# Kernel optimization log

Hardware: AMD Instinct MI355X
Metric: run time of the kernel (lower is better)

The kernel has to match this reference:

```python
import jax, jax.numpy as jnp
import numpy as np

B, S, E, H, G = 2, 2048, 2048, 16, 4
D = E // H  # head dim = 128


def setup_inputs() -> dict:
    key = jax.random.key(0)
    ks = jax.random.split(key, 7)
    scale = 1.0 / np.sqrt(E)
    x = jax.random.normal(ks[0], (B, S, E), dtype=jnp.float32)
    Wq = jax.random.normal(ks[1], (H, E, D), dtype=jnp.float32) * scale
    bq = jax.random.normal(ks[2], (H, D), dtype=jnp.float32) * 0.02
    Wk = jax.random.normal(ks[3], (G, E, D), dtype=jnp.float32) * scale
    bk = jax.random.normal(ks[4], (G, D), dtype=jnp.float32) * 0.02
    Wv = jax.random.normal(ks[5], (G, E, D), dtype=jnp.float32) * scale
    bv = jax.random.normal(ks[6], (G, D), dtype=jnp.float32) * 0.02
    return {"x": x, "Wq": Wq, "bq": bq, "Wk": Wk, "bk": bk, "Wv": Wv, "bv": bv}


def reference(x, Wq, bq, Wk, bk, Wv, bv):
    # x: [B,S,E]; Wq: [H,E,D]; Wk/Wv: [G,E,D]
    h, e, d = Wq.shape
    g = Wk.shape[0]
    per = h // g  # Q heads per KV group
    s = x.shape[1]

    # batched QKV projections (replaces per-head nn.Linear loop)
    q = jnp.einsum('bse,hed->bhsd', x, Wq) + bq[None, :, None, :]   # [B,H,S,D]
    kg = jnp.einsum('bse,ged->bgsd', x, Wk) + bk[None, :, None, :]  # [B,G,S,D]
    vg = jnp.einsum('bse,ged->bgsd', x, Wv) + bv[None, :, None, :]

    # GQA: each KV group serves `per` consecutive Q heads (order i*per+j)
    k = jnp.repeat(kg, per, axis=1)  # [B,H,S,D]
    v = jnp.repeat(vg, per, axis=1)

    scores = jnp.einsum('bhqd,bhkd->bhqk', q, k) * (1.0 / np.sqrt(d))
    causal = jnp.triu(jnp.ones((s, s), dtype=bool), k=1)  # strict upper = masked
    scores = jnp.where(causal[None, None, :, :], -jnp.inf, scores)
    attn = jax.nn.softmax(scores, axis=-1)
    out = jnp.einsum('bhqk,bhkd->bhqd', attn, v)  # [B,H,S,D]
    # concat per-head outputs along feature dim (head order matches loop order)
    return out.transpose(0, 2, 1, 3).reshape(x.shape[0], s, h * d)
```

## Files before the change

kernel.cpp:

```cpp
#include <hip/hip_runtime.h>
#include <hip/hip_bf16.h>
#include <math.h>


typedef __attribute__((ext_vector_type(8))) short bf16x8;
typedef __attribute__((ext_vector_type(4))) short s16x4;
typedef __attribute__((ext_vector_type(4))) float f32x4;
typedef __attribute__((ext_vector_type(16))) float f32x16;

#define LOG2E 1.4426950408889634f

__device__ __forceinline__ short f2bf(float f) {
  union { float f; unsigned u; } v; v.f = f;
  unsigned r = v.u + 0x7FFFu + ((v.u >> 16) & 1u);
  return (short)(r >> 16);
}

__device__ __forceinline__ short hwbf(float f) {
  __hip_bfloat16 h = __float2bfloat16(f);
  return *(short*)&h;
}

__device__ __forceinline__ unsigned pkbf(float a, float b) {
  return (unsigned)(unsigned short)hwbf(a) | ((unsigned)(unsigned short)hwbf(b) << 16);
}

__device__ __forceinline__ void async16(const void* g, void* l) {
  __builtin_amdgcn_global_load_lds(
      (const __attribute__((address_space(1))) void*)g,
      (__attribute__((address_space(3))) void*)l, 16, 0, 0);
}

__device__ __forceinline__ f32x4 mfma16(bf16x8 a, bf16x8 b, f32x4 c) {
  return __builtin_amdgcn_mfma_f32_16x16x32_bf16(a, b, c, 0, 0, 0);
}

__device__ __forceinline__ f32x16 mfma32(bf16x8 a, bf16x8 b, f32x16 c) {
  return __builtin_amdgcn_mfma_f32_32x32x16_bf16(a, b, c, 0, 0, 0);
}


__global__ void conv_x(const float4* __restrict__ x, s16x4* __restrict__ xb) {
  const int i = blockIdx.x * 256 + threadIdx.x;
  float4 v = x[i];
  s16x4 o;
  o[0] = f2bf(v.x); o[1] = f2bf(v.y); o[2] = f2bf(v.z); o[3] = f2bf(v.w);
  xb[i] = o;
}

__global__ void transpose_w(const float* __restrict__ src, short* __restrict__ wt, int c0) {
  __shared__ float t[32][33];
  const int hh = blockIdx.z;
  const int e0 = blockIdx.x * 32, d0 = blockIdx.y * 32;
  const int tx = threadIdx.x, ty = threadIdx.y;
  const float* s = src + (size_t)hh * 2048 * 128;
#pragma unroll
  for (int i = ty; i < 32; i += 8)
    t[i][tx] = s[(size_t)(e0 + i) * 128 + d0 + tx];
  __syncthreads();
#pragma unroll
  for (int i = ty; i < 32; i += 8)
    wt[(size_t)(c0 + hh * 128 + d0 + i) * 2048 + e0 + tx] = f2bf(t[tx][i]);
}

__global__ void build_bias(const float* __restrict__ bq, const float* __restrict__ bk,
                           const float* __restrict__ bv, float* __restrict__ bc) {
  const int c = blockIdx.x * 256 + threadIdx.x;
  float v;
  if (c < 2048)      v = bq[c];
  else if (c < 2560) v = bk[c - 2048];
  else               v = bv[c - 2560];
  bc[c] = v;
}


__global__ __launch_bounds__(256) void qkv_gemm(
    const short* __restrict__ xb, const short* __restrict__ wt,
    const float* __restrict__ bc,
    short* __restrict__ qb, short* __restrict__ kb, short* __restrict__ vt)
{
  constexpr int E = 2048, BK = 32;
  __shared__ short Al[2][128 * BK];
  __shared__ short Bl[2][128 * BK];
  const int tid = threadIdx.x;
  const int lane = tid & 63, wave = tid >> 6;
  const int wr = wave >> 1, wc = wave & 1;
  const int l16 = lane & 15, grp = lane >> 4;
  const int work = (blockIdx.x & 7) * 96 + (blockIdx.x >> 3);
  const int m0 = (work / 24) * 128, n0 = (work % 24) * 128;

  const int c1 = tid, c2 = tid + 256;
  const int r1 = c1 >> 2, s1 = c1 & 3, r2 = c2 >> 2, s2 = c2 & 3;

  f32x4 acc[4][4] = {};

  async16(xb + (size_t)(m0 + r1) * E + s1 * 8, (char*)Al[0] + c1 * 16);
  async16(xb + (size_t)(m0 + r2) * E + s2 * 8, (char*)Al[0] + c2 * 16);
  async16(wt + (size_t)(n0 + r1) * E + s1 * 8, (char*)Bl[0] + c1 * 16);
  async16(wt + (size_t)(n0 + r2) * E + s2 * 8, (char*)Bl[0] + c2 * 16);
  __syncthreads();

  const int nk = E / BK;
  for (int t = 0; t < nk; ++t) {
    const int cur = t & 1;
    if (t + 1 < nk) {
      const int k0 = (t + 1) * BK;
      async16(xb + (size_t)(m0 + r1) * E + k0 + s1 * 8, (char*)Al[cur ^ 1] + c1 * 16);
      async16(xb + (size_t)(m0 + r2) * E + k0 + s2 * 8, (char*)Al[cur ^ 1] + c2 * 16);
      async16(wt + (size_t)(n0 + r1) * E + k0 + s1 * 8, (char*)Bl[cur ^ 1] + c1 * 16);
      async16(wt + (size_t)(n0 + r2) * E + k0 + s2 * 8, (char*)Bl[cur ^ 1] + c2 * 16);
    }
    bf16x8 af[4], bfr[4];
#pragma unroll
    for (int mi = 0; mi < 4; ++mi)
      af[mi] = *(const bf16x8*)&Al[cur][(wr * 64 + mi * 16 + l16) * BK + grp * 8];
#pragma unroll
    for (int ni = 0; ni < 4; ++ni)
      bfr[ni] = *(const bf16x8*)&Bl[cur][(wc * 64 + ni * 16 + l16) * BK + grp * 8];
#pragma unroll
    for (int mi = 0; mi < 4; ++mi)
#pragma unroll
      for (int ni = 0; ni < 4; ++ni)
        acc[mi][ni] = mfma16(af[mi], bfr[ni], acc[mi][ni]);
    __syncthreads();
  }

  const float qscale = 0.08838834764831845f;
#pragma unroll
  for (int ni = 0; ni < 4; ++ni) {
    const int c = n0 + wc * 64 + ni * 16 + l16;
    const float bias = bc[c];
    const int d = c & 127;
#pragma unroll
    for (int mi = 0; mi < 4; ++mi) {
      const int rbase = m0 + wr * 64 + mi * 16 + grp * 4;
      const int b = rbase >> 11;
      const int s = rbase & 2047;
      f32x4 a = acc[mi][ni];
      if (c < 2048) {
        const int h = c >> 7;
        short* dst = qb + ((size_t)(b * 16 + h) * 2048 + s) * 128 + d;
#pragma unroll
        for (int r = 0; r < 4; ++r) dst[(size_t)r * 128] = f2bf((a[r] + bias) * qscale);
      } else if (c < 2560) {
        const int gi = (c >> 7) & 3;
        short* dst = kb + ((size_t)(b * 4 + gi) * 2048 + s) * 128 + d;
#pragma unroll
        for (int r = 0; r < 4; ++r) dst[(size_t)r * 128] = f2bf(a[r] + bias);
      } else {
        const int gi = (c >> 7) & 3;
        s16x4 pk;
#pragma unroll
        for (int r = 0; r < 4; ++r) pk[r] = f2bf(a[r] + bias);
        const int vcol = (s & ~12) | ((s & 4) << 1) | ((s & 8) >> 1);
        *(s16x4*)&vt[((size_t)(b * 4 + gi) * 128 + d) * 2048 + vcol] = pk;
      }
    }
  }
}


__device__ __forceinline__ void stageKV(char* kd, char* vd,
                                        const short* __restrict__ Kg,
                                        const short* __restrict__ Vg,
                                        int kv0, int tid) {
#pragma unroll
  for (int rd = 0; rd < 4; ++rd) {
    const int off = rd * 4096 + tid * 16;
    const int row = off >> 8, colb = off & 255;
    const int sc = colb ^ ((row & 15) << 4);
    async16(Kg + (size_t)(kv0 + row) * 128 + (sc >> 1), kd + off);
  }
#pragma unroll
  for (int rd = 0; rd < 4; ++rd) {
    const int off = rd * 4096 + tid * 16;
    const int row = off >> 7, colb = off & 127;
    const int sc = colb ^ ((row & 7) << 4);
    async16(Vg + (size_t)row * 2048 + kv0 + (sc >> 1), vd + off);
  }
}

__global__ __launch_bounds__(256) void attn(
    const short* __restrict__ qb, const short* __restrict__ kb,
    const short* __restrict__ vt, float* __restrict__ out)
{
  constexpr int S = 2048, D = 128;
  extern __shared__ char lds[];
  const int tid = threadIdx.x;
  const int lane = tid & 63, wave = tid >> 6;
  const int l32 = lane & 31;
  const int hhf = lane >> 5;
  const int swzK = (l32 & 15) << 4;
  const int swzV = (l32 & 7) << 4;
  const int work = (blockIdx.x & 7) * 32 + (blockIdx.x >> 3);
  const int bg = work >> 5;
  const int b = bg >> 2, g = bg & 3;
  const int h = g * 4 + ((work >> 3) & 3);
  const int x = work & 7;

  const short* Qg = qb + (size_t)(b * 16 + h) * S * D;
  const short* Kg = kb + (size_t)(b * 4 + g) * S * D;
  const short* Vg = vt + (size_t)(b * 4 + g) * (size_t)D * S;

#pragma unroll
  for (int p = 0; p < 2; ++p) {
    const int jj = p ? (15 - x) : x;
    const int q0 = jj * 128 + wave * 32;
    const int nt = 2 * (jj + 1);

    bf16x8 qf[8];
#pragma unroll
    for (int c = 0; c < 8; ++c)
      qf[c] = *(const bf16x8*)&Qg[(size_t)(q0 + l32) * D + c * 16 + hhf * 8];

    f32x16 o[4] = {};
    float mrun = -INFINITY, lrun = 0.f;

    stageKV(lds, lds + 32768, Kg, Vg, 0, tid);
    __syncthreads();

    for (int t = 0; t < nt; ++t) {
      const int kv0 = t << 6;
      const int cur = t & 1;
      if (t + 1 < nt)
        stageKV(lds + (cur ^ 1) * 16384, lds + 32768 + (cur ^ 1) * 16384,
                Kg, Vg, kv0 + 64, tid);
      const char* Kb = lds + cur * 16384;
      const char* Vb = lds + 32768 + cur * 16384;

      if (kv0 <= q0 + 31) {
        f32x16 st[2] = {};
        __builtin_amdgcn_s_setprio(1);
#pragma unroll
        for (int c = 0; c < 8; ++c) {
          const int X = c * 32 + hhf * 16;
          bf16x8 k0 = *(const bf16x8*)(Kb + (size_t)l32 * 256 + (X ^ swzK));
          st[0] = mfma32(k0, qf[c], st[0]);
          bf16x8 k1 = *(const bf16x8*)(Kb + (size_t)(32 + l32) * 256 + (X ^ swzK));
          st[1] = mfma32(k1, qf[c], st[1]);
        }
        __builtin_amdgcn_s_setprio(0);

        if (kv0 + 63 > q0) {
          const int qa = q0 + l32;
#pragma unroll
          for (int r = 0; r < 16; ++r) {
            const int kl = (r & 3) + 8 * (r >> 2) + 4 * hhf;
            if (kv0 + kl > qa)      st[0][r] = -INFINITY;
            if (kv0 + 32 + kl > qa) st[1][r] = -INFINITY;
          }
        }

        float tmax = -INFINITY;
#pragma unroll
        for (int r = 0; r < 16; ++r) {
          tmax = fmaxf(tmax, st[0][r]);
          tmax = fmaxf(tmax, st[1][r]);
        }
        tmax = fmaxf(tmax, __shfl_xor(tmax, 32));
        float fac = 1.0f;
        if (!__all(tmax <= mrun + 8.0f)) {
          const float mn = fmaxf(mrun, tmax);
          fac = exp2f((mrun - mn) * LOG2E);
#pragma unroll
          for (int db = 0; db < 4; ++db) o[db] *= fac;
          mrun = mn;
        }
        float lsum = 0.f;
        float ps0[16], ps1[16];
#pragma unroll
        for (int r = 0; r < 16; ++r) {
          ps0[r] = exp2f((st[0][r] - mrun) * LOG2E); lsum += ps0[r];
          ps1[r] = exp2f((st[1][r] - mrun) * LOG2E); lsum += ps1[r];
        }
        lsum += __shfl_xor(lsum, 32);
        lrun = lrun * fac + lsum;

        bf16x8 pf[4];
#pragma unroll
        for (int kbi = 0; kbi < 4; ++kbi) {
          union { unsigned u[4]; bf16x8 v; } tu;
          const int c0 = 8 * (kbi & 1);
          if (kbi < 2) {
            tu.u[0] = pkbf(ps0[c0 + 0], ps0[c0 + 1]);
            tu.u[1] = pkbf(ps0[c0 + 2], ps0[c0 + 3]);
            tu.u[2] = pkbf(ps0[c0 + 4], ps0[c0 + 5]);
            tu.u[3] = pkbf(ps0[c0 + 6], ps0[c0 + 7]);
          } else {
            tu.u[0] = pkbf(ps1[c0 + 0], ps1[c0 + 1]);
            tu.u[1] = pkbf(ps1[c0 + 2], ps1[c0 + 3]);
            tu.u[2] = pkbf(ps1[c0 + 4], ps1[c0 + 5]);
            tu.u[3] = pkbf(ps1[c0 + 6], ps1[c0 + 7]);
          }
          pf[kbi] = tu.v;
        }

        __builtin_amdgcn_s_setprio(1);
#pragma unroll
        for (int kbi = 0; kbi < 4; ++kbi) {
          const int X = kbi * 32 + hhf * 16;
#pragma unroll
          for (int db = 0; db < 4; ++db) {
            bf16x8 vf = *(const bf16x8*)(Vb + (size_t)(db * 32 + l32) * 128 + (X ^ swzV));
            o[db] = mfma32(vf, pf[kbi], o[db]);
          }
        }
        __builtin_amdgcn_s_setprio(0);
      }
      __syncthreads();
    }

    const float inv = 1.f / lrun;
    float* orow = out + ((size_t)b * S + q0 + l32) * 2048 + h * D;
#pragma unroll
    for (int db = 0; db < 4; ++db)
#pragma unroll
      for (int rq = 0; rq < 4; ++rq) {
        f32x4 w;
        w[0] = o[db][4 * rq + 0] * inv;
        w[1] = o[db][4 * rq + 1] * inv;
        w[2] = o[db][4 * rq + 2] * inv;
        w[3] = o[db][4 * rq + 3] * inv;
        *(f32x4*)&orow[db * 32 + 8 * rq + 4 * hhf] = w;
      }
  }
}


extern "C" void kernel_launch(void* const* d_in, const int* in_sizes, int n_in,
                              void* d_out, int out_size, void* d_ws, size_t ws_size,
                              hipStream_t stream) {
  const float* x  = (const float*)d_in[0];
  const float* Wq = (const float*)d_in[1];
  const float* bq = (const float*)d_in[2];
  const float* Wk = (const float*)d_in[3];
  const float* bk = (const float*)d_in[4];
  const float* Wv = (const float*)d_in[5];
  const float* bv = (const float*)d_in[6];
  float* out = (float*)d_out;

  char* ws = (char*)d_ws;
  short* xb = (short*)ws;
  short* wt = (short*)(ws + (size_t)16 * 1024 * 1024);
  float* bc = (float*)(ws + (size_t)28 * 1024 * 1024);
  short* qb = (short*)(ws + (size_t)28 * 1024 * 1024 + 65536);
  short* kb = (short*)((char*)qb + (size_t)16 * 1024 * 1024);
  short* vt = (short*)((char*)kb + (size_t)4 * 1024 * 1024);

  conv_x<<<8192, 256, 0, stream>>>((const float4*)x, (s16x4*)xb);
  dim3 tb(32, 8);
  transpose_w<<<dim3(64, 4, 16), tb, 0, stream>>>(Wq, wt, 0);
  transpose_w<<<dim3(64, 4, 4),  tb, 0, stream>>>(Wk, wt, 2048);
  transpose_w<<<dim3(64, 4, 4),  tb, 0, stream>>>(Wv, wt, 2560);
  build_bias<<<12, 256, 0, stream>>>(bq, bk, bv, bc);
  qkv_gemm<<<768, 256, 0, stream>>>(xb, wt, bc, qb, kb, vt);

  (void)hipFuncSetAttribute((const void*)attn, hipFuncAttributeMaxDynamicSharedMemorySize, 65536);
  attn<<<256, 256, 65536, stream>>>(qb, kb, vt, out);
}
```

Before: 267.2 us.

## Triple-buffer K/V tiles in attention with explicit vmcnt waits

Moves the attention kernel's K/V LDS staging from double to triple buffering. Tiles are now prefetched two iterations ahead, and __syncthreads is replaced by raw s_barrier plus partial s_waitcnt vmcnt counts, so the next tile's global loads can stay in flight while the current tile is consumed. This is meant to hide global memory latency better. In exchange LDS use grows from 64KB to 96KB per block, and correctness now depends on hand-counted outstanding-load numbers.

```diff
diff --git a/kernel.cpp b/kernel.cpp
--- a/kernel.cpp
+++ b/kernel.cpp
@@ -160,7 +160,7 @@
 }
 
 
-__device__ __forceinline__ void stageKV(char* kd, char* vd,
+__device__ __forceinline__ void stageKV(char* set,
                                         const short* __restrict__ Kg,
                                         const short* __restrict__ Vg,
                                         int kv0, int tid) {
@@ -169,14 +169,14 @@
     const int off = rd * 4096 + tid * 16;
     const int row = off >> 8, colb = off & 255;
     const int sc = colb ^ ((row & 15) << 4);
-    async16(Kg + (size_t)(kv0 + row) * 128 + (sc >> 1), kd + off);
+    async16(Kg + (size_t)(kv0 + row) * 128 + (sc >> 1), set + off);
   }
 #pragma unroll
   for (int rd = 0; rd < 4; ++rd) {
     const int off = rd * 4096 + tid * 16;
     const int row = off >> 7, colb = off & 127;
     const int sc = colb ^ ((row & 7) << 4);
-    async16(Vg + (size_t)row * 2048 + kv0 + (sc >> 1), vd + off);
+    async16(Vg + (size_t)row * 2048 + kv0 + (sc >> 1), set + 16384 + off);
   }
 }
 
@@ -216,17 +216,28 @@
     f32x16 o[4] = {};
     float mrun = -INFINITY, lrun = 0.f;
 
-    stageKV(lds, lds + 32768, Kg, Vg, 0, tid);
-    __syncthreads();
-
+    __builtin_amdgcn_s_barrier();
+    stageKV(lds, Kg, Vg, 0, tid);
+    stageKV(lds + 32768, Kg, Vg, 64, tid);
+
+    int cb = 0;
+    int sb = 2;
     for (int t = 0; t < nt; ++t) {
       const int kv0 = t << 6;
-      const int cur = t & 1;
-      if (t + 1 < nt)
-        stageKV(lds + (cur ^ 1) * 16384, lds + 32768 + (cur ^ 1) * 16384,
-                Kg, Vg, kv0 + 64, tid);
-      const char* Kb = lds + cur * 16384;
-      const char* Vb = lds + 32768 + cur * 16384;
+      __builtin_amdgcn_s_barrier();
+      if (t + 2 < nt) {
+        stageKV(lds + sb * 32768, Kg, Vg, kv0 + 128, tid);
+        asm volatile("s_waitcnt vmcnt(16)" ::: "memory");
+      } else if (t + 1 < nt) {
+        asm volatile("s_waitcnt vmcnt(8)" ::: "memory");
+      } else {
+        asm volatile("s_waitcnt vmcnt(0)" ::: "memory");
+      }
+      __builtin_amdgcn_s_barrier();
+      __builtin_amdgcn_sched_barrier(0);
+
+      const char* Kb = lds + cb * 32768;
+      const char* Vb = lds + cb * 32768 + 16384;
 
       if (kv0 <= q0 + 31) {
         f32x16 st[2] = {};
@@ -307,7 +318,8 @@
         }
         __builtin_amdgcn_s_setprio(0);
       }
-      __syncthreads();
+      cb = (cb == 2) ? 0 : cb + 1;
+      sb = (sb == 2) ? 0 : sb + 1;
     }
 
     const float inv = 1.f / lrun;
@@ -355,6 +367,6 @@
   build_bias<<<12, 256, 0, stream>>>(bq, bk, bv, bc);
   qkv_gemm<<<768, 256, 0, stream>>>(xb, wt, bc, qb, kb, vt);
 
-  (void)hipFuncSetAttribute((const void*)attn, hipFuncAttributeMaxDynamicSharedMemorySize, 65536);
-  attn<<<256, 256, 65536, stream>>>(qb, kb, vt, out);
-}
+  (void)hipFuncSetAttribute((const void*)attn, hipFuncAttributeMaxDynamicSharedMemorySize, 98304);
+  attn<<<256, 256, 98304, stream>>>(qb, kb, vt, out);
+}
```

Measured after the change: 267.2 us. About the same (-0.0%).
